# Performance work log

Hardware: AMD Instinct MI355X
Metric: run time of the kernel (lower is better)

## Reference

```python
import jax, jax.numpy as jnp
import numpy as np

C = 256      # in_channels
NH = 4       # n_heads
NG = 32      # GroupNorm num_groups
EPS = 1e-5   # torch GroupNorm default eps


def _conv1x1(x, w, b):
    # 1x1 conv == per-pixel channel matmul. x: (B,C,H,W), w: (O,C), b: (O,)
    return jnp.einsum('oc,bchw->bohw', w, x) + b[None, :, None, None]


def _groupnorm(x, gamma, beta):
    b, c, h, w = x.shape
    xg = x.reshape(b, NG, c // NG, h, w)
    mu = xg.mean(axis=(2, 3, 4), keepdims=True)
    var = xg.var(axis=(2, 3, 4), keepdims=True)
    xn = ((xg - mu) * jax.lax.rsqrt(var + EPS)).reshape(b, c, h, w)
    return xn * gamma[None, :, None, None] + beta[None, :, None, None]


def setup_inputs() -> dict:
    key = jax.random.key(0)
    ks = jax.random.split(key, 5)
    B, H, W = 2, 64, 64
    s = 1.0 / np.sqrt(C).astype(np.float32)
    return {
        'x': jax.random.normal(ks[0], (B, C, H, W), jnp.float32),
        'gamma': jnp.ones((C,), jnp.float32),
        'beta': jnp.zeros((C,), jnp.float32),
        'wq': jax.random.normal(ks[1], (C, C), jnp.float32) * s,
        'bq': jnp.zeros((C,), jnp.float32),
        'wk': jax.random.normal(ks[2], (C, C), jnp.float32) * s,
        'bk': jnp.zeros((C,), jnp.float32),
        'wv': jax.random.normal(ks[3], (C, C), jnp.float32) * s,
        'bv': jnp.zeros((C,), jnp.float32),
        'wp': jax.random.normal(ks[4], (C, C), jnp.float32) * s,
        'bp': jnp.zeros((C,), jnp.float32),
    }


def reference(x, gamma, beta, wq, bq, wk, bk, wv, bv, wp, bp):
    b, c, h, w = x.shape
    c_ = c // NH  # head dim
    hn = _groupnorm(x, gamma, beta)
    # NOTE: original splits channels as (head_dim, n_heads) with head_dim leading
    q = _conv1x1(hn, wq, bq).reshape(b, c_, NH, h * w)
    k = _conv1x1(hn, wk, bk).reshape(b, c_, NH, h * w)
    v = _conv1x1(hn, wv, bv).reshape(b, c_, NH, h * w)
    scores = jnp.einsum('bcnq,bcnk->bqkn', q, k) * (c_ ** -0.5)  # (B,S,S,NH)
    attn = jax.nn.softmax(scores, axis=2)  # softmax over key axis
    out = jnp.einsum('bcnd,bqdn->bcnq', v, attn).reshape(b, c, h, w)
    return x + _conv1x1(out, wp, bp)
```

## Files before the change

### kernel.cpp

```cpp
#include <hip/hip_runtime.h>

#define CH 256
#define NHEAD 4
#define HD 64
#define SP 4096
#define NB 2
#define QSCALE 0.1803368801111204f

typedef __attribute__((ext_vector_type(8))) short bf16x8;
typedef __attribute__((ext_vector_type(4))) float f32x4;
typedef unsigned int u32;
typedef unsigned short u16;

__device__ inline u16 b16(float f) {
    u32 u = __float_as_uint(f);
    return (u16)((u + 0x8000u) >> 16);
}
__device__ inline float fexp2(float x) { return __builtin_amdgcn_exp2f(x); }

__global__ __launch_bounds__(256) void prep_kernel(
    const float* __restrict__ x, float2* __restrict__ part,
    const float* __restrict__ wq, const float* __restrict__ wk,
    const float* __restrict__ wv, const float* __restrict__ wp,
    u16* __restrict__ wqb, u16* __restrict__ wkb,
    u16* __restrict__ wvb, u16* __restrict__ wpb)
{
    int tid = threadIdx.x;
    if (blockIdx.x < 256) {
        int bgq = blockIdx.x;
        int bg = bgq >> 2, qtr = bgq & 3;
        const float4* xp = (const float4*)(x + (size_t)bg * 8 * SP) + qtr * 2048;
        float s = 0.f, ss = 0.f;
        for (int i = tid; i < 2048; i += 256) {
            float4 u = xp[i];
            s  += (u.x + u.y) + (u.z + u.w);
            ss += (u.x * u.x + u.y * u.y) + (u.z * u.z + u.w * u.w);
        }
#pragma unroll
        for (int off = 32; off > 0; off >>= 1) {
            s  += __shfl_down(s, off);
            ss += __shfl_down(ss, off);
        }
        __shared__ float ws_s[4], ws_q[4];
        int w = tid >> 6;
        if ((tid & 63) == 0) { ws_s[w] = s; ws_q[w] = ss; }
        __syncthreads();
        if (tid == 0)
            part[bgq] = make_float2(ws_s[0] + ws_s[1] + ws_s[2] + ws_s[3],
                                    ws_q[0] + ws_q[1] + ws_q[2] + ws_q[3]);
    } else {
        int idx = (blockIdx.x - 256) * 256 + tid;
        int m = idx >> 16, i = idx & 65535;
        if (m == 0)      wqb[i] = b16(wq[i] * QSCALE);
        else if (m == 1) wkb[i] = b16(wk[i]);
        else if (m == 2) wvb[i] = b16(wv[i]);
        else {
            int c = i >> 8, chan = i & 255;
            int n = chan >> 6, d = chan & 63;
            wpb[i] = b16(wp[c * 256 + d * 4 + n]);
        }
    }
}

__global__ __launch_bounds__(256) void xprep_kernel(
    const float* __restrict__ x, const float2* __restrict__ part,
    const float* __restrict__ gamma, const float* __restrict__ beta,
    u16* __restrict__ xt)
{
    int b = blockIdx.z, c0 = blockIdx.y * 64, s0 = blockIdx.x * 64;
    int tid = threadIdx.x;
    __shared__ u16 Lt[64][72];
    int cl = tid >> 2, sg = tid & 3;
    int c = c0 + cl;
    int bg = b * 32 + (c >> 3);
    float s = 0.f, ss = 0.f;
#pragma unroll
    for (int q = 0; q < 4; q++) { float2 p = part[bg * 4 + q]; s += p.x; ss += p.y; }
    float mu = s * (1.f / 32768.f);
    float var = ss * (1.f / 32768.f) - mu * mu;
    float rs = rsqrtf(var + 1e-5f);
    float ga = gamma[c];
    float aa = rs * ga, bb = beta[c] - mu * rs * ga;

    const float* xr = x + ((size_t)b * CH + c) * SP + s0 + sg * 16;
#pragma unroll
    for (int i = 0; i < 4; i++) {
        float4 v = *(const float4*)&xr[4 * i];
        int sl = sg * 16 + 4 * i;
        Lt[sl + 0][cl] = b16(fmaf(aa, v.x, bb));
        Lt[sl + 1][cl] = b16(fmaf(aa, v.y, bb));
        Lt[sl + 2][cl] = b16(fmaf(aa, v.z, bb));
        Lt[sl + 3][cl] = b16(fmaf(aa, v.w, bb));
    }
    __syncthreads();
    int sl = tid >> 2, ch = (tid & 3) * 2;
    u16* dst = xt + ((size_t)b * SP + s0 + sl) * CH + c0;
    *(uint4*)&dst[ch * 8]       = *(const uint4*)&Lt[sl][ch * 8];
    *(uint4*)&dst[(ch + 1) * 8] = *(const uint4*)&Lt[sl][(ch + 1) * 8];
}

__global__ __launch_bounds__(256) void qkv_gemm_kernel(
    const u16* __restrict__ xt, const u16* __restrict__ wqb,
    const u16* __restrict__ wkb, const u16* __restrict__ wvb,
    const float* __restrict__ bq, const float* __restrict__ bk,
    const float* __restrict__ bv,
    u16* __restrict__ qt, u16* __restrict__ ktp, u16* __restrict__ vtp)
{
    int zz = blockIdx.y;
    int b = zz / 3, p = zz % 3;
    const u16* W = (p == 0) ? wqb : (p == 1) ? wkb : wvb;
    const float* bias = (p == 0) ? bq : (p == 1) ? bk : bv;
    float bs = (p == 0) ? QSCALE : 1.f;
    int s0 = blockIdx.x * 32;
    int tid = threadIdx.x, w = tid >> 6, lane = tid & 63;
    int t = lane >> 4, ln = lane & 15;

    __shared__ u16 Ts[10240];

    f32x4 acc[4][2];
#pragma unroll
    for (int og = 0; og < 4; og++)
#pragma unroll
        for (int sg = 0; sg < 2; sg++)
            acc[og][sg] = (f32x4){0.f, 0.f, 0.f, 0.f};

    const u16* xb = xt + ((size_t)b * SP + s0) * CH;

#pragma unroll
    for (int ks = 0; ks < 8; ks++) {
        bf16x8 af[4], bf[2];
#pragma unroll
        for (int og = 0; og < 4; og++)
            af[og] = *(const bf16x8*)&W[(size_t)(w * 64 + og * 16 + ln) * CH + ks * 32 + t * 8];
#pragma unroll
        for (int sg = 0; sg < 2; sg++)
            bf[sg] = *(const bf16x8*)&xb[(size_t)(sg * 16 + ln) * CH + ks * 32 + t * 8];
#pragma unroll
        for (int og = 0; og < 4; og++)
#pragma unroll
            for (int sg = 0; sg < 2; sg++)
                acc[og][sg] = __builtin_amdgcn_mfma_f32_16x16x32_bf16(
                    af[og], bf[sg], acc[og][sg], 0, 0, 0);
    }

    if (p < 2) {
#pragma unroll
        for (int og = 0; og < 4; og++)
#pragma unroll
            for (int sg = 0; sg < 2; sg++)
#pragma unroll
                for (int r = 0; r < 4; r++) {
                    int o = w * 64 + og * 16 + 4 * t + r;
                    Ts[(r * 32 + sg * 16 + ln) * 72 + (w * 16 + og * 4 + t)] =
                        b16(acc[og][sg][r] + bias[o] * bs);
                }
        __syncthreads();
        if (p == 0) {
#pragma unroll
            for (int it = 0; it < 4; it++) {
                int idx = it * 256 + tid;
                int o8 = idx & 7, sl = (idx >> 3) & 31, n = idx >> 8;
                *(uint4*)&qt[((size_t)(b * 4 + n) * SP + s0 + sl) * HD + o8 * 8] =
                    *(const uint4*)&Ts[(n * 32 + sl) * 72 + o8 * 8];
            }
        } else {
#pragma unroll
            for (int it = 0; it < 4; it++) {
                int idx = it * 256 + tid;
                int o8 = idx & 7, sl = (idx >> 3) & 31, n = idx >> 8;
                int key = s0 + sl;
                int g = ((key >> 4) & 3) * 2 + (o8 >> 2);
                int lp = (key & 15) + 16 * (o8 & 3);
                *(uint4*)&ktp[(size_t)(b * 4 + n) * SP * HD +
                              (size_t)(key >> 6) * 4096 + g * 512 + lp * 8] =
                    *(const uint4*)&Ts[(n * 32 + sl) * 72 + o8 * 8];
            }
        }
    } else {
#pragma unroll
        for (int og = 0; og < 4; og++)
#pragma unroll
            for (int sg = 0; sg < 2; sg++)
#pragma unroll
                for (int r = 0; r < 4; r++) {
                    int o = w * 64 + og * 16 + 4 * t + r;
                    Ts[(r * 64 + w * 16 + og * 4 + t) * 40 + sg * 16 + ln] =
                        b16(acc[og][sg][r] + bias[o]);
                }
        __syncthreads();
#pragma unroll
        for (int it = 0; it < 4; it++) {
            int idx = it * 256 + tid;
            int so8 = idx & 3, d = (idx >> 2) & 63, n = idx >> 8;
            int key = s0 + so8 * 8;
            int g = ((d >> 4) & 3) * 2 + ((key >> 5) & 1);
            int lp = (d & 15) + 16 * ((key >> 3) & 3);
            *(uint4*)&vtp[(size_t)(b * 4 + n) * SP * HD +
                          (size_t)(key >> 6) * 4096 + g * 512 + lp * 8] =
                *(const uint4*)&Ts[(n * 64 + d) * 40 + so8 * 8];
        }
    }
}

__global__ __launch_bounds__(256, 4) void attn_kernel(
    const u16* __restrict__ qtb, const u16* __restrict__ ktp,
    const u16* __restrict__ vtp, u16* __restrict__ opart,
    float* __restrict__ lpart)
{
    int bx = blockIdx.x;
    int z = bx & 7, qt_i = (bx >> 3) & 31, sp = bx >> 8;
    int sq0 = qt_i * 128;
    int tile0 = sp * 16;
    const u16* qz = qtb + (size_t)z * SP * HD;
    const u16* kz = ktp + (size_t)z * SP * HD;
    const u16* vz = vtp + (size_t)z * SP * HD;

    int tid = threadIdx.x, w = tid >> 6, l = tid & 63;
    int t = l >> 4, ln = l & 15;

    __shared__ __align__(16) u16 Kb[2][4096];
    __shared__ __align__(16) u16 Vb[4096];
    __shared__ __align__(16) u32 Pb[4][2][512];

    bf16x8 qf[2][2];
#pragma unroll
    for (int qg = 0; qg < 2; qg++)
#pragma unroll
        for (int ds = 0; ds < 2; ds++)
            qf[qg][ds] = *(const bf16x8*)&qz[
                (size_t)(sq0 + w * 32 + qg * 16 + ln) * HD + ds * 32 + t * 8];

    uint4 kr[2], vr[2];
#pragma unroll
    for (int gi = 0; gi < 2; gi++) {
        int g = 2 * w + gi;
        kr[gi] = *(const uint4*)&kz[(size_t)tile0 * 4096 + g * 512 + l * 8];
        vr[gi] = *(const uint4*)&vz[(size_t)tile0 * 4096 + g * 512 + l * 8];
    }
#pragma unroll
    for (int gi = 0; gi < 2; gi++) {
        int g = 2 * w + gi;
        *(uint4*)&Kb[0][g * 512 + l * 8] = kr[gi];
        *(uint4*)&Vb[g * 512 + l * 8] = vr[gi];
    }

    float lsum[2] = {0.f, 0.f};
    f32x4 oacc[2][4];
#pragma unroll
    for (int qg = 0; qg < 2; qg++)
#pragma unroll
        for (int dg = 0; dg < 4; dg++)
            oacc[qg][dg] = (f32x4){0.f, 0.f, 0.f, 0.f};

    const f32x4 z4 = {0.f, 0.f, 0.f, 0.f};
    f32x4 sa[2][4];

    auto ep = [&](int qg) {
#pragma unroll
        for (int kg = 0; kg < 4; kg++) {
            float e0 = fexp2(sa[qg][kg][0]);
            float e1 = fexp2(sa[qg][kg][1]);
            float e2 = fexp2(sa[qg][kg][2]);
            float e3 = fexp2(sa[qg][kg][3]);
            lsum[qg] += (e0 + e1) + (e2 + e3);
            u32 p0 = __builtin_amdgcn_perm(__float_as_uint(e1), __float_as_uint(e0), 0x07060302u);
            u32 p1 = __builtin_amdgcn_perm(__float_as_uint(e3), __float_as_uint(e2), 0x07060302u);
            int Lt = ln + 16 * (2 * (kg & 1) + (t >> 1));
            int ksg = kg >> 1;
            *(uint2*)&Pb[w][qg][(ksg * 64 + Lt) * 4 + 2 * (t & 1)] =
                make_uint2(p0, p1);
        }
    };

    for (int kti = 0; kti < 16; kti++) {
        int cb = kti & 1;
        __syncthreads();

        if (kti < 15) {
            size_t nb = (size_t)(tile0 + kti + 1) * 4096;
#pragma unroll
            for (int gi = 0; gi < 2; gi++) {
                int g = 2 * w + gi;
                kr[gi] = *(const uint4*)&kz[nb + g * 512 + l * 8];
                vr[gi] = *(const uint4*)&vz[nb + g * 512 + l * 8];
            }
        }

#pragma unroll
        for (int kg = 0; kg < 4; kg++) {
            bf16x8 kf = *(const bf16x8*)&Kb[cb][(kg * 2 + 0) * 512 + l * 8];
#pragma unroll
            for (int qg = 0; qg < 2; qg++)
                sa[qg][kg] = __builtin_amdgcn_mfma_f32_16x16x32_bf16(
                    kf, qf[qg][0], z4, 0, 0, 0);
        }
#pragma unroll
        for (int kg = 0; kg < 4; kg++) {
            bf16x8 kf = *(const bf16x8*)&Kb[cb][(kg * 2 + 1) * 512 + l * 8];
#pragma unroll
            for (int qg = 0; qg < 2; qg++)
                sa[qg][kg] = __builtin_amdgcn_mfma_f32_16x16x32_bf16(
                    kf, qf[qg][1], sa[qg][kg], 0, 0, 0);
        }

        if (kti < 15) {
#pragma unroll
            for (int gi = 0; gi < 2; gi++) {
                int g = 2 * w + gi;
                *(uint4*)&Kb[1 - cb][g * 512 + l * 8] = kr[gi];
            }
        }

        ep(0);
#pragma unroll
        for (int qg = 0; qg < 2; qg++) {
            if (qg == 0) ep(1);
            bf16x8 pf[2];
#pragma unroll
            for (int ksg = 0; ksg < 2; ksg++)
                pf[ksg] = *(const bf16x8*)&Pb[w][qg][(ksg * 64 + l) * 4];
#pragma unroll
            for (int ksg = 0; ksg < 2; ksg++)
#pragma unroll
                for (int dg = 0; dg < 4; dg++) {
                    bf16x8 vf = *(const bf16x8*)&Vb[(dg * 2 + ksg) * 512 + l * 8];
                    oacc[qg][dg] = __builtin_amdgcn_mfma_f32_16x16x32_bf16(
                        pf[ksg], vf, oacc[qg][dg], 0, 0, 0);
                }
        }

        __syncthreads();
        if (kti < 15) {
#pragma unroll
            for (int gi = 0; gi < 2; gi++) {
                int g = 2 * w + gi;
                *(uint4*)&Vb[g * 512 + l * 8] = vr[gi];
            }
        }
    }

#pragma unroll
    for (int qg = 0; qg < 2; qg++) {
        lsum[qg] += __shfl_xor(lsum[qg], 16);
        lsum[qg] += __shfl_xor(lsum[qg], 32);
    }

    size_t obase = (size_t)(sp * 8 + z) * SP;
#pragma unroll
    for (int qg = 0; qg < 2; qg++)
#pragma unroll
        for (int dg = 0; dg < 4; dg++)
#pragma unroll
            for (int r = 0; r < 4; r++) {
                int q = sq0 + w * 32 + qg * 16 + 4 * t + r;
                opart[(obase + q) * HD + dg * 16 + ln] = b16(oacc[qg][dg][r]);
            }
    if (t == 0)
#pragma unroll
        for (int qg = 0; qg < 2; qg++)
            lpart[obase + sq0 + w * 32 + qg * 16 + ln] = lsum[qg];
}

__global__ __launch_bounds__(256) void combine_kernel(
    const u16* __restrict__ opart, const float* __restrict__ lpart,
    u16* __restrict__ ot)
{
    int z = blockIdx.x;
    int q0 = blockIdx.y * 32;
    int tid = threadIdx.x;
    int q = q0 + (tid >> 3), dq = tid & 7;
    int b = z >> 2, n = z & 3;
    float acc[8] = {0.f, 0.f, 0.f, 0.f, 0.f, 0.f, 0.f, 0.f};
    float lt = 0.f;
#pragma unroll
    for (int sp = 0; sp < 4; sp++) {
        size_t base = (size_t)(sp * 8 + z) * SP + q;
        uint4 a = *(const uint4*)&opart[base * HD + dq * 8];
        lt += lpart[base];
        u32 av[4] = {a.x, a.y, a.z, a.w};
#pragma unroll
        for (int i = 0; i < 4; i++) {
            acc[2 * i + 0] += __uint_as_float(av[i] << 16);
            acc[2 * i + 1] += __uint_as_float(av[i] & 0xffff0000u);
        }
    }
    float inv = 1.f / lt;
    u32 res[4];
#pragma unroll
    for (int i = 0; i < 4; i++) {
        u16 rl = b16(acc[2 * i + 0] * inv);
        u16 rh = b16(acc[2 * i + 1] * inv);
        res[i] = ((u32)rh << 16) | rl;
    }
    *(uint4*)&ot[((size_t)b * SP + q) * CH + n * 64 + dq * 8] =
        make_uint4(res[0], res[1], res[2], res[3]);
}

__global__ __launch_bounds__(256) void proj_gemm_kernel(
    const u16* __restrict__ ot, const u16* __restrict__ wpb,
    const float* __restrict__ bp, const float* __restrict__ x,
    float* __restrict__ out)
{
    int b = blockIdx.y;
    int s0 = blockIdx.x * 16;
    int tid = threadIdx.x, w = tid >> 6, lane = tid & 63;
    int t = lane >> 4, ln = lane & 15;

    f32x4 acc[4];
#pragma unroll
    for (int og = 0; og < 4; og++)
        acc[og] = (f32x4){0.f, 0.f, 0.f, 0.f};

    const u16* ob = ot + ((size_t)b * SP + s0) * CH;

#pragma unroll
    for (int ks = 0; ks < 8; ks++) {
        bf16x8 af[4];
#pragma unroll
        for (int og = 0; og < 4; og++)
            af[og] = *(const bf16x8*)&wpb[(size_t)(w * 64 + og * 16 + ln) * CH + ks * 32 + t * 8];
        bf16x8 bf = *(const bf16x8*)&ob[(size_t)ln * CH + ks * 32 + t * 8];
#pragma unroll
        for (int og = 0; og < 4; og++)
            acc[og] = __builtin_amdgcn_mfma_f32_16x16x32_bf16(
                af[og], bf, acc[og], 0, 0, 0);
    }

#pragma unroll
    for (int og = 0; og < 4; og++)
#pragma unroll
        for (int r = 0; r < 4; r++) {
            int c = w * 64 + og * 16 + 4 * t + r;
            size_t idx = ((size_t)b * CH + c) * SP + s0 + ln;
            out[idx] = acc[og][r] + bp[c] + x[idx];
        }
}

extern "C" void kernel_launch(void* const* d_in, const int* in_sizes, int n_in,
                              void* d_out, int out_size, void* d_ws, size_t ws_size,
                              hipStream_t stream)
{
    const float* x     = (const float*)d_in[0];
    const float* gamma = (const float*)d_in[1];
    const float* beta  = (const float*)d_in[2];
    const float* wq = (const float*)d_in[3]; const float* bq = (const float*)d_in[4];
    const float* wk = (const float*)d_in[5]; const float* bk = (const float*)d_in[6];
    const float* wv = (const float*)d_in[7]; const float* bv = (const float*)d_in[8];
    const float* wp = (const float*)d_in[9]; const float* bp = (const float*)d_in[10];
    float* out = (float*)d_out;

    const size_t TEN = (size_t)8 * SP * HD;
    char* wsb = (char*)d_ws;
    float2* part = (float2*)wsb;
    u16* wqb = (u16*)(wsb + 4096);
    u16* wkb = wqb + 65536;
    u16* wvb = wkb + 65536;
    u16* wpb = wvb + 65536;
    u16* qt  = wpb + 65536;
    u16* ktp = qt + TEN;
    u16* vtp = ktp + TEN;
    u16* xt  = vtp + TEN;
    u16* ot  = xt;
    u16* opart = xt + TEN;
    float* lpart = (float*)(opart + 4 * TEN);

    prep_kernel<<<dim3(1280), dim3(256), 0, stream>>>(
        x, part, wq, wk, wv, wp, wqb, wkb, wvb, wpb);
    xprep_kernel<<<dim3(64, 4, 2), dim3(256), 0, stream>>>(x, part, gamma, beta, xt);
    qkv_gemm_kernel<<<dim3(128, 6), dim3(256), 0, stream>>>(
        xt, wqb, wkb, wvb, bq, bk, bv, qt, ktp, vtp);
    attn_kernel<<<dim3(1024), dim3(256), 0, stream>>>(qt, ktp, vtp, opart, lpart);
    combine_kernel<<<dim3(8, 128), dim3(256), 0, stream>>>(opart, lpart, ot);
    proj_gemm_kernel<<<dim3(256, 2), dim3(256), 0, stream>>>(ot, wpb, bp, x, out);
}
```

Measured before the change: 175.0 us.

## Fuse norm into QKV GEMM, combine into projection, register-resident K/V in attention

The GroupNorm apply and transpose move into the QKV GEMM, which stages normalized x in shared memory, so the xt round trip and one launch go away. The split-KV combine is folded into the projection GEMM, which sums the four partials and normalizes on the fly. The attention kernel drops LDS staging and barriers for K/V, loading them straight from global into registers (occupancy hint lowered to 3), and writes its output through LDS for coalesced stores. The trade-offs are higher register pressure in attention, redundant reads of x across the three q/k/v blocks, and repeated partial reads in the projection.

Result: faster. 159.8 us (-8.6%).

```diff
diff --git a/kernel.cpp b/kernel.cpp
--- a/kernel.cpp
+++ b/kernel.cpp
@@ -62,46 +62,11 @@
     }
 }
 
-__global__ __launch_bounds__(256) void xprep_kernel(
+__global__ __launch_bounds__(256) void qkv_gemm_kernel(
     const float* __restrict__ x, const float2* __restrict__ part,
     const float* __restrict__ gamma, const float* __restrict__ beta,
-    u16* __restrict__ xt)
-{
-    int b = blockIdx.z, c0 = blockIdx.y * 64, s0 = blockIdx.x * 64;
-    int tid = threadIdx.x;
-    __shared__ u16 Lt[64][72];
-    int cl = tid >> 2, sg = tid & 3;
-    int c = c0 + cl;
-    int bg = b * 32 + (c >> 3);
-    float s = 0.f, ss = 0.f;
-#pragma unroll
-    for (int q = 0; q < 4; q++) { float2 p = part[bg * 4 + q]; s += p.x; ss += p.y; }
-    float mu = s * (1.f / 32768.f);
-    float var = ss * (1.f / 32768.f) - mu * mu;
-    float rs = rsqrtf(var + 1e-5f);
-    float ga = gamma[c];
-    float aa = rs * ga, bb = beta[c] - mu * rs * ga;
-
-    const float* xr = x + ((size_t)b * CH + c) * SP + s0 + sg * 16;
-#pragma unroll
-    for (int i = 0; i < 4; i++) {
-        float4 v = *(const float4*)&xr[4 * i];
-        int sl = sg * 16 + 4 * i;
-        Lt[sl + 0][cl] = b16(fmaf(aa, v.x, bb));
-        Lt[sl + 1][cl] = b16(fmaf(aa, v.y, bb));
-        Lt[sl + 2][cl] = b16(fmaf(aa, v.z, bb));
-        Lt[sl + 3][cl] = b16(fmaf(aa, v.w, bb));
-    }
-    __syncthreads();
-    int sl = tid >> 2, ch = (tid & 3) * 2;
-    u16* dst = xt + ((size_t)b * SP + s0 + sl) * CH + c0;
-    *(uint4*)&dst[ch * 8]       = *(const uint4*)&Lt[sl][ch * 8];
-    *(uint4*)&dst[(ch + 1) * 8] = *(const uint4*)&Lt[sl][(ch + 1) * 8];
-}
-
-__global__ __launch_bounds__(256) void qkv_gemm_kernel(
-    const u16* __restrict__ xt, const u16* __restrict__ wqb,
-    const u16* __restrict__ wkb, const u16* __restrict__ wvb,
+    const u16* __restrict__ wqb, const u16* __restrict__ wkb,
+    const u16* __restrict__ wvb,
     const float* __restrict__ bq, const float* __restrict__ bk,
     const float* __restrict__ bv,
     u16* __restrict__ qt, u16* __restrict__ ktp, u16* __restrict__ vtp)
@@ -115,7 +80,38 @@
     int tid = threadIdx.x, w = tid >> 6, lane = tid & 63;
     int t = lane >> 4, ln = lane & 15;
 
-    __shared__ u16 Ts[10240];
+    __shared__ u16 SB[10240];
+    __shared__ float As[256], Bs[256];
+
+    {
+        int c = tid, bg = b * 32 + (c >> 3);
+        float s = 0.f, ss = 0.f;
+#pragma unroll
+        for (int q = 0; q < 4; q++) { float2 pp = part[bg * 4 + q]; s += pp.x; ss += pp.y; }
+        float mu = s * (1.f / 32768.f);
+        float var = ss * (1.f / 32768.f) - mu * mu;
+        float rs = rsqrtf(var + 1e-5f);
+        float ga = gamma[c];
+        As[c] = rs * ga;
+        Bs[c] = beta[c] - mu * rs * ga;
+    }
+    __syncthreads();
+
+    {
+        int cb = tid >> 3;
+        int sseg = (tid & 7) * 4;
+#pragma unroll
+        for (int it = 0; it < 8; it++) {
+            int c = it * 32 + cb;
+            float4 v = *(const float4*)&x[((size_t)b * CH + c) * SP + s0 + sseg];
+            float aa = As[c], bb = Bs[c];
+            SB[(sseg + 0) * 264 + c] = b16(fmaf(aa, v.x, bb));
+            SB[(sseg + 1) * 264 + c] = b16(fmaf(aa, v.y, bb));
+            SB[(sseg + 2) * 264 + c] = b16(fmaf(aa, v.z, bb));
+            SB[(sseg + 3) * 264 + c] = b16(fmaf(aa, v.w, bb));
+        }
+    }
+    __syncthreads();
 
     f32x4 acc[4][2];
 #pragma unroll
@@ -124,24 +120,23 @@
         for (int sg = 0; sg < 2; sg++)
             acc[og][sg] = (f32x4){0.f, 0.f, 0.f, 0.f};
 
-    const u16* xb = xt + ((size_t)b * SP + s0) * CH;
-
 #pragma unroll
     for (int ks = 0; ks < 8; ks++) {
-        bf16x8 af[4], bf[2];
+        bf16x8 af[4], bfv[2];
 #pragma unroll
         for (int og = 0; og < 4; og++)
             af[og] = *(const bf16x8*)&W[(size_t)(w * 64 + og * 16 + ln) * CH + ks * 32 + t * 8];
 #pragma unroll
         for (int sg = 0; sg < 2; sg++)
-            bf[sg] = *(const bf16x8*)&xb[(size_t)(sg * 16 + ln) * CH + ks * 32 + t * 8];
+            bfv[sg] = *(const bf16x8*)&SB[(sg * 16 + ln) * 264 + ks * 32 + t * 8];
 #pragma unroll
         for (int og = 0; og < 4; og++)
 #pragma unroll
             for (int sg = 0; sg < 2; sg++)
                 acc[og][sg] = __builtin_amdgcn_mfma_f32_16x16x32_bf16(
-                    af[og], bf[sg], acc[og][sg], 0, 0, 0);
-    }
+                    af[og], bfv[sg], acc[og][sg], 0, 0, 0);
+    }
+    __syncthreads();
 
     if (p < 2) {
 #pragma unroll
@@ -151,7 +146,7 @@
 #pragma unroll
                 for (int r = 0; r < 4; r++) {
                     int o = w * 64 + og * 16 + 4 * t + r;
-                    Ts[(r * 32 + sg * 16 + ln) * 72 + (w * 16 + og * 4 + t)] =
+                    SB[(r * 32 + sg * 16 + ln) * 72 + (w * 16 + og * 4 + t)] =
                         b16(acc[og][sg][r] + bias[o] * bs);
                 }
         __syncthreads();
@@ -161,7 +156,7 @@
                 int idx = it * 256 + tid;
                 int o8 = idx & 7, sl = (idx >> 3) & 31, n = idx >> 8;
                 *(uint4*)&qt[((size_t)(b * 4 + n) * SP + s0 + sl) * HD + o8 * 8] =
-                    *(const uint4*)&Ts[(n * 32 + sl) * 72 + o8 * 8];
+                    *(const uint4*)&SB[(n * 32 + sl) * 72 + o8 * 8];
             }
         } else {
 #pragma unroll
@@ -173,7 +168,7 @@
                 int lp = (key & 15) + 16 * (o8 & 3);
                 *(uint4*)&ktp[(size_t)(b * 4 + n) * SP * HD +
                               (size_t)(key >> 6) * 4096 + g * 512 + lp * 8] =
-                    *(const uint4*)&Ts[(n * 32 + sl) * 72 + o8 * 8];
+                    *(const uint4*)&SB[(n * 32 + sl) * 72 + o8 * 8];
             }
         }
     } else {
@@ -184,7 +179,7 @@
 #pragma unroll
                 for (int r = 0; r < 4; r++) {
                     int o = w * 64 + og * 16 + 4 * t + r;
-                    Ts[(r * 64 + w * 16 + og * 4 + t) * 40 + sg * 16 + ln] =
+                    SB[(r * 64 + w * 16 + og * 4 + t) * 40 + sg * 16 + ln] =
                         b16(acc[og][sg][r] + bias[o]);
                 }
         __syncthreads();
@@ -197,12 +192,12 @@
             int lp = (d & 15) + 16 * ((key >> 3) & 3);
             *(uint4*)&vtp[(size_t)(b * 4 + n) * SP * HD +
                           (size_t)(key >> 6) * 4096 + g * 512 + lp * 8] =
-                *(const uint4*)&Ts[(n * 64 + d) * 40 + so8 * 8];
-        }
-    }
-}
-
-__global__ __launch_bounds__(256, 4) void attn_kernel(
+                *(const uint4*)&SB[(n * 64 + d) * 40 + so8 * 8];
+        }
+    }
+}
+
+__global__ __launch_bounds__(256, 3) void attn_kernel(
     const u16* __restrict__ qtb, const u16* __restrict__ ktp,
     const u16* __restrict__ vtp, u16* __restrict__ opart,
     float* __restrict__ lpart)
@@ -218,8 +213,6 @@
     int tid = threadIdx.x, w = tid >> 6, l = tid & 63;
     int t = l >> 4, ln = l & 15;
 
-    __shared__ __align__(16) u16 Kb[2][4096];
-    __shared__ __align__(16) u16 Vb[4096];
     __shared__ __align__(16) u32 Pb[4][2][512];
 
     bf16x8 qf[2][2];
@@ -230,19 +223,10 @@
             qf[qg][ds] = *(const bf16x8*)&qz[
                 (size_t)(sq0 + w * 32 + qg * 16 + ln) * HD + ds * 32 + t * 8];
 
-    uint4 kr[2], vr[2];
-#pragma unroll
-    for (int gi = 0; gi < 2; gi++) {
-        int g = 2 * w + gi;
-        kr[gi] = *(const uint4*)&kz[(size_t)tile0 * 4096 + g * 512 + l * 8];
-        vr[gi] = *(const uint4*)&vz[(size_t)tile0 * 4096 + g * 512 + l * 8];
-    }
-#pragma unroll
-    for (int gi = 0; gi < 2; gi++) {
-        int g = 2 * w + gi;
-        *(uint4*)&Kb[0][g * 512 + l * 8] = kr[gi];
-        *(uint4*)&Vb[g * 512 + l * 8] = vr[gi];
-    }
+    bf16x8 kf[8], vf[8];
+#pragma unroll
+    for (int g = 0; g < 8; g++)
+        kf[g] = *(const bf16x8*)&kz[(size_t)tile0 * 4096 + g * 512 + l * 8];
 
     float lsum[2] = {0.f, 0.f};
     f32x4 oacc[2][4];
@@ -273,42 +257,32 @@
     };
 
     for (int kti = 0; kti < 16; kti++) {
-        int cb = kti & 1;
-        __syncthreads();
-
-        if (kti < 15) {
-            size_t nb = (size_t)(tile0 + kti + 1) * 4096;
-#pragma unroll
-            for (int gi = 0; gi < 2; gi++) {
-                int g = 2 * w + gi;
-                kr[gi] = *(const uint4*)&kz[nb + g * 512 + l * 8];
-                vr[gi] = *(const uint4*)&vz[nb + g * 512 + l * 8];
-            }
-        }
+        size_t tb = (size_t)(tile0 + kti) * 4096;
+
+#pragma unroll
+        for (int g = 0; g < 8; g++)
+            vf[g] = *(const bf16x8*)&vz[tb + g * 512 + l * 8];
 
 #pragma unroll
         for (int kg = 0; kg < 4; kg++) {
-            bf16x8 kf = *(const bf16x8*)&Kb[cb][(kg * 2 + 0) * 512 + l * 8];
 #pragma unroll
             for (int qg = 0; qg < 2; qg++)
                 sa[qg][kg] = __builtin_amdgcn_mfma_f32_16x16x32_bf16(
-                    kf, qf[qg][0], z4, 0, 0, 0);
+                    kf[kg * 2 + 0], qf[qg][0], z4, 0, 0, 0);
         }
 #pragma unroll
         for (int kg = 0; kg < 4; kg++) {
-            bf16x8 kf = *(const bf16x8*)&Kb[cb][(kg * 2 + 1) * 512 + l * 8];
 #pragma unroll
             for (int qg = 0; qg < 2; qg++)
                 sa[qg][kg] = __builtin_amdgcn_mfma_f32_16x16x32_bf16(
-                    kf, qf[qg][1], sa[qg][kg], 0, 0, 0);
+                    kf[kg * 2 + 1], qf[qg][1], sa[qg][kg], 0, 0, 0);
         }
 
         if (kti < 15) {
-#pragma unroll
-            for (int gi = 0; gi < 2; gi++) {
-                int g = 2 * w + gi;
-                *(uint4*)&Kb[1 - cb][g * 512 + l * 8] = kr[gi];
-            }
+            size_t nb = tb + 4096;
+#pragma unroll
+            for (int g = 0; g < 8; g++)
+                kf[g] = *(const bf16x8*)&kz[nb + g * 512 + l * 8];
         }
 
         ep(0);
@@ -322,20 +296,9 @@
 #pragma unroll
             for (int ksg = 0; ksg < 2; ksg++)
 #pragma unroll
-                for (int dg = 0; dg < 4; dg++) {
-                    bf16x8 vf = *(const bf16x8*)&Vb[(dg * 2 + ksg) * 512 + l * 8];
+                for (int dg = 0; dg < 4; dg++)
                     oacc[qg][dg] = __builtin_amdgcn_mfma_f32_16x16x32_bf16(
-                        pf[ksg], vf, oacc[qg][dg], 0, 0, 0);
-                }
-        }
-
-        __syncthreads();
-        if (kti < 15) {
-#pragma unroll
-            for (int gi = 0; gi < 2; gi++) {
-                int g = 2 * w + gi;
-                *(uint4*)&Vb[g * 512 + l * 8] = vr[gi];
-            }
+                        pf[ksg], vf[dg * 2 + ksg], oacc[qg][dg], 0, 0, 0);
         }
     }
 
@@ -346,84 +309,85 @@
     }
 
     size_t obase = (size_t)(sp * 8 + z) * SP;
+    u16* po = (u16*)&Pb[w][0][0];
 #pragma unroll
     for (int qg = 0; qg < 2; qg++)
 #pragma unroll
         for (int dg = 0; dg < 4; dg++)
 #pragma unroll
-            for (int r = 0; r < 4; r++) {
-                int q = sq0 + w * 32 + qg * 16 + 4 * t + r;
-                opart[(obase + q) * HD + dg * 16 + ln] = b16(oacc[qg][dg][r]);
-            }
+            for (int r = 0; r < 4; r++)
+                po[(qg * 16 + 4 * t + r) * 64 + dg * 16 + ln] = b16(oacc[qg][dg][r]);
+#pragma unroll
+    for (int i = 0; i < 4; i++) {
+        int f = i * 512 + l * 8;
+        int qloc = f >> 6, d0 = f & 63;
+        uint4 v = *(const uint4*)&po[f];
+        *(uint4*)&opart[(obase + sq0 + w * 32 + qloc) * HD + d0] = v;
+    }
     if (t == 0)
 #pragma unroll
         for (int qg = 0; qg < 2; qg++)
             lpart[obase + sq0 + w * 32 + qg * 16 + ln] = lsum[qg];
 }
 
-__global__ __launch_bounds__(256) void combine_kernel(
+__global__ __launch_bounds__(256) void proj_gemm_kernel(
     const u16* __restrict__ opart, const float* __restrict__ lpart,
-    u16* __restrict__ ot)
-{
-    int z = blockIdx.x;
-    int q0 = blockIdx.y * 32;
-    int tid = threadIdx.x;
-    int q = q0 + (tid >> 3), dq = tid & 7;
-    int b = z >> 2, n = z & 3;
-    float acc[8] = {0.f, 0.f, 0.f, 0.f, 0.f, 0.f, 0.f, 0.f};
-    float lt = 0.f;
-#pragma unroll
-    for (int sp = 0; sp < 4; sp++) {
-        size_t base = (size_t)(sp * 8 + z) * SP + q;
-        uint4 a = *(const uint4*)&opart[base * HD + dq * 8];
-        lt += lpart[base];
-        u32 av[4] = {a.x, a.y, a.z, a.w};
-#pragma unroll
-        for (int i = 0; i < 4; i++) {
-            acc[2 * i + 0] += __uint_as_float(av[i] << 16);
-            acc[2 * i + 1] += __uint_as_float(av[i] & 0xffff0000u);
-        }
-    }
-    float inv = 1.f / lt;
-    u32 res[4];
-#pragma unroll
-    for (int i = 0; i < 4; i++) {
-        u16 rl = b16(acc[2 * i + 0] * inv);
-        u16 rh = b16(acc[2 * i + 1] * inv);
-        res[i] = ((u32)rh << 16) | rl;
-    }
-    *(uint4*)&ot[((size_t)b * SP + q) * CH + n * 64 + dq * 8] =
-        make_uint4(res[0], res[1], res[2], res[3]);
-}
-
-__global__ __launch_bounds__(256) void proj_gemm_kernel(
-    const u16* __restrict__ ot, const u16* __restrict__ wpb,
-    const float* __restrict__ bp, const float* __restrict__ x,
-    float* __restrict__ out)
+    const u16* __restrict__ wpb, const float* __restrict__ bp,
+    const float* __restrict__ x, float* __restrict__ out)
 {
     int b = blockIdx.y;
     int s0 = blockIdx.x * 16;
     int tid = threadIdx.x, w = tid >> 6, lane = tid & 63;
     int t = lane >> 4, ln = lane & 15;
 
+    float linv[4];
+#pragma unroll
+    for (int n = 0; n < 4; n++) {
+        float s = 0.f;
+#pragma unroll
+        for (int sp = 0; sp < 4; sp++)
+            s += lpart[(size_t)(sp * 8 + b * 4 + n) * SP + s0 + ln];
+        linv[n] = 1.f / s;
+    }
+
     f32x4 acc[4];
 #pragma unroll
     for (int og = 0; og < 4; og++)
         acc[og] = (f32x4){0.f, 0.f, 0.f, 0.f};
 
-    const u16* ob = ot + ((size_t)b * SP + s0) * CH;
-
 #pragma unroll
     for (int ks = 0; ks < 8; ks++) {
         bf16x8 af[4];
 #pragma unroll
         for (int og = 0; og < 4; og++)
             af[og] = *(const bf16x8*)&wpb[(size_t)(w * 64 + og * 16 + ln) * CH + ks * 32 + t * 8];
-        bf16x8 bf = *(const bf16x8*)&ob[(size_t)ln * CH + ks * 32 + t * 8];
+
+        int n = ks >> 1;
+        int d0 = (ks & 1) * 32 + t * 8;
+        u32 ov[4][4];
+#pragma unroll
+        for (int sp = 0; sp < 4; sp++) {
+            uint4 o4 = *(const uint4*)&opart[
+                ((size_t)(sp * 8 + b * 4 + n) * SP + s0 + ln) * HD + d0];
+            ov[sp][0] = o4.x; ov[sp][1] = o4.y; ov[sp][2] = o4.z; ov[sp][3] = o4.w;
+        }
+        float inv = linv[n];
+        union { u32 u[4]; bf16x8 v; } bu;
+#pragma unroll
+        for (int i = 0; i < 4; i++) {
+            float lo = 0.f, hi = 0.f;
+#pragma unroll
+            for (int sp = 0; sp < 4; sp++) {
+                lo += __uint_as_float(ov[sp][i] << 16);
+                hi += __uint_as_float(ov[sp][i] & 0xffff0000u);
+            }
+            u16 rl = b16(lo * inv), rh = b16(hi * inv);
+            bu.u[i] = ((u32)rh << 16) | rl;
+        }
 #pragma unroll
         for (int og = 0; og < 4; og++)
             acc[og] = __builtin_amdgcn_mfma_f32_16x16x32_bf16(
-                af[og], bf, acc[og], 0, 0, 0);
+                af[og], bu.v, acc[og], 0, 0, 0);
     }
 
 #pragma unroll
@@ -459,17 +423,14 @@
     u16* qt  = wpb + 65536;
     u16* ktp = qt + TEN;
     u16* vtp = ktp + TEN;
-    u16* xt  = vtp + TEN;
-    u16* ot  = xt;
-    u16* opart = xt + TEN;
+    u16* opart = vtp + TEN;
     float* lpart = (float*)(opart + 4 * TEN);
 
     prep_kernel<<<dim3(1280), dim3(256), 0, stream>>>(
         x, part, wq, wk, wv, wp, wqb, wkb, wvb, wpb);
-    xprep_kernel<<<dim3(64, 4, 2), dim3(256), 0, stream>>>(x, part, gamma, beta, xt);
     qkv_gemm_kernel<<<dim3(128, 6), dim3(256), 0, stream>>>(
-        xt, wqb, wkb, wvb, bq, bk, bv, qt, ktp, vtp);
+        x, part, gamma, beta, wqb, wkb, wvb, bq, bk, bv, qt, ktp, vtp);
     attn_kernel<<<dim3(1024), dim3(256), 0, stream>>>(qt, ktp, vtp, opart, lpart);
-    combine_kernel<<<dim3(8, 128), dim3(256), 0, stream>>>(opart, lpart, ot);
-    proj_gemm_kernel<<<dim3(256, 2), dim3(256), 0, stream>>>(ot, wpb, bp, x, out);
-}
+    proj_gemm_kernel<<<dim3(256, 2), dim3(256), 0, stream>>>(
+        opart, lpart, wpb, bp, x, out);
+}
```
